# Performance work log

Hardware: AMD Instinct MI355X
Metric: run time of the kernel (lower is better)

Reference implementation:

```python
import jax, jax.numpy as jnp
import numpy as np

B, N, C = 32, 577, 768
H = 12
DH = C // H  # 64
SCALE = DH ** -0.5


def setup_inputs() -> dict:
    key = jax.random.key(0)
    ks = jax.random.split(key, 5)
    x = jax.random.normal(ks[0], (B, N, C), dtype=jnp.float32)
    # Linear params (torch convention: y = x @ W.T + b)
    qkv_w = jax.random.normal(ks[1], (3 * C, C), dtype=jnp.float32) * (C ** -0.5)
    qkv_b = jnp.zeros((3 * C,), dtype=jnp.float32)
    proj_w = jax.random.normal(ks[2], (C, C), dtype=jnp.float32) * (C ** -0.5)
    proj_b = jnp.zeros((C,), dtype=jnp.float32)
    return {"x": x, "qkv_w": qkv_w, "qkv_b": qkv_b, "proj_w": proj_w, "proj_b": proj_b}


def reference(x, qkv_w, qkv_b, proj_w, proj_b):
    b, n, c = x.shape
    qkv = x @ qkv_w.T + qkv_b                       # [B, N, 3C]
    qkv = qkv.reshape(b, n, 3, H, DH).transpose(2, 0, 3, 1, 4)  # [3, B, H, N, DH]
    q, k, v = qkv[0], qkv[1], qkv[2]
    q = q * SCALE
    attn = jnp.einsum('bhnd,bhmd->bhnm', q, k)      # [B, H, N, N]
    # sigmoid -> inverse-sigmoid straight-through rewrite (forward equals logit(sigmoid(attn)))
    sig = jax.nn.sigmoid(attn)
    inv_sig = jnp.log(sig / (1.0 - sig))
    attn_st = attn + jax.lax.stop_gradient(inv_sig - attn)
    p = jax.nn.softmax(attn_st, axis=-1)
    out = jnp.einsum('bhnm,bhmd->bhnd', p, v)       # [B, H, N, DH]
    out = out.transpose(0, 2, 1, 3).reshape(b, n, c)
    return out @ proj_w.T + proj_b
```

## Files before the change

kernel.cpp:

```cpp
#include <hip/hip_runtime.h>

typedef __bf16 bf16;
typedef __attribute__((ext_vector_type(4))) __bf16 bf16x4;
typedef __attribute__((ext_vector_type(8))) __bf16 bf16x8;
typedef __attribute__((ext_vector_type(4))) float f32x4;

#define MFMA_BF16(A_, B_, C_) __builtin_amdgcn_mfma_f32_16x16x32_bf16(A_, B_, C_, 0, 0, 0)

#define BB    32
#define SEQ   577
#define CH    768
#define NH    12
#define DHD   64
#define MROWS (BB * SEQ)
#define NQKV  2304
#define SEQP  584
#define QSCALE 0.1803368801111204f

#define NSTEP 24

__device__ __forceinline__ int xcd_chunk(int bid, int nwg) {
  int q8 = nwg >> 3, r8 = nwg & 7;
  int xcd = bid & 7, sub = bid >> 3;
  return (xcd < r8 ? xcd * (q8 + 1) : r8 * (q8 + 1) + (xcd - r8) * q8) + sub;
}

__device__ __forceinline__ void async_ld16(const bf16* g, bf16* l) {
  __builtin_amdgcn_global_load_lds(
      (const __attribute__((address_space(1))) void*)g,
      (__attribute__((address_space(3))) void*)l, 16, 0, 0);
}

__global__ __launch_bounds__(256) void cvt_bf16(const float* __restrict__ src,
                                                bf16* __restrict__ dst, int n) {
  int idx = (blockIdx.x * 256 + threadIdx.x) * 4;
  if (idx >= n) return;
  float4 v = *(const float4*)(src + idx);
  bf16x4 o = {(bf16)v.x, (bf16)v.y, (bf16)v.z, (bf16)v.w};
  *(bf16x4*)(dst + idx) = o;
}

__global__ __launch_bounds__(256) void pad_v(bf16* __restrict__ vt) {
  int r = blockIdx.x * 256 + threadIdx.x;
  if (r < BB * NH * DHD) {
    bf16* p = vt + (size_t)r * SEQP + SEQ;
#pragma unroll
    for (int i = 0; i < 7; ++i) p[i] = (bf16)0.f;
  }
}

__global__ __launch_bounds__(256, 2)
void gemm_qkv(const bf16* __restrict__ A, const bf16* __restrict__ W,
              const float* __restrict__ bias,
              bf16* __restrict__ qrm, bf16* __restrict__ krm, bf16* __restrict__ vt) {
  __shared__ bf16 As[2][128 * 32];
  __shared__ bf16 Bs[2][128 * 32];
  const int tid = threadIdx.x, lane = tid & 63, wid = tid >> 6;
  const int quad = lane >> 4, r15 = lane & 15;
  const int m0 = blockIdx.y * 128, n0 = blockIdx.x * 128;
  const int waveM = wid & 1, waveN = wid >> 1;

  const bf16* aSrc[2];
  const bf16* bSrc[2];
  for (int c = 0; c < 2; ++c) {
    int q = wid * 128 + c * 64 + lane;
    int row = q >> 2;
    int sw = (row ^ (row >> 2)) & 3;
    int kc = (q & 3) ^ sw;
    aSrc[c] = A + (size_t)(m0 + row) * CH + kc * 8;
    bSrc[c] = W + (size_t)(n0 + row) * CH + kc * 8;
  }

  f32x4 acc[4][4];
#pragma unroll
  for (int i = 0; i < 4; ++i)
#pragma unroll
    for (int j = 0; j < 4; ++j) acc[i][j] = (f32x4){0.f, 0.f, 0.f, 0.f};

#define GSTAGE(K0, BUF)                                                   \
  {                                                                       \
    _Pragma("unroll") for (int c = 0; c < 2; ++c) {                       \
      async_ld16(aSrc[c] + (K0), &As[BUF][(wid * 128 + c * 64) * 8]);     \
      async_ld16(bSrc[c] + (K0), &Bs[BUF][(wid * 128 + c * 64) * 8]);     \
    }                                                                     \
  }

#define GCOMPUTE(BUF)                                                     \
  {                                                                       \
    bf16x8 af[4], bfr[4];                                                 \
    _Pragma("unroll") for (int s = 0; s < 4; ++s) {                       \
      int rowA = waveM * 64 + s * 16 + r15;                               \
      int ca = quad ^ ((rowA ^ (rowA >> 2)) & 3);                         \
      af[s] = *(const bf16x8*)(&As[BUF][rowA * 32 + ca * 8]);             \
      int rowB = waveN * 64 + s * 16 + r15;                               \
      int cb = quad ^ ((rowB ^ (rowB >> 2)) & 3);                         \
      bfr[s] = *(const bf16x8*)(&Bs[BUF][rowB * 32 + cb * 8]);            \
    }                                                                     \
    _Pragma("unroll") for (int sm = 0; sm < 4; ++sm)                      \
      _Pragma("unroll") for (int sn = 0; sn < 4; ++sn)                    \
        acc[sm][sn] = MFMA_BF16(af[sm], bfr[sn], acc[sm][sn]);            \
  }

  GSTAGE(0, 0);
  for (int k0 = 0; k0 < CH; k0 += 64) {
    __syncthreads();
    GSTAGE(k0 + 32, 1);
    GCOMPUTE(0);
    __syncthreads();
    if (k0 + 64 < CH) GSTAGE(k0 + 64, 0);
    GCOMPUTE(1);
  }

  int t = (n0 >= 1536) ? 2 : (n0 >= 768 ? 1 : 0);
#pragma unroll
  for (int sn = 0; sn < 4; ++sn) {
    int gn = n0 + waveN * 64 + sn * 16 + r15;
    float bv = bias[gn];
    int col = gn - t * CH;
    int h = col >> 6, d = col & 63;
#pragma unroll
    for (int sm = 0; sm < 4; ++sm) {
      int gmBase = m0 + waveM * 64 + sm * 16 + quad * 4;
#pragma unroll
      for (int r = 0; r < 4; ++r) {
        int gm = gmBase + r;
        if (gm < MROWS) {
          float v = acc[sm][sn][r] + bv;
          if (t == 0) {
            qrm[(size_t)gm * CH + col] = (bf16)(v * QSCALE);
          } else if (t == 1) {
            krm[(size_t)gm * CH + col] = (bf16)v;
          } else {
            int b_ = gm / SEQ;
            int n_ = gm - b_ * SEQ;
            vt[((size_t)(b_ * NH + h) * DHD + d) * SEQP + n_] = (bf16)v;
          }
        }
      }
    }
  }
}
#undef GSTAGE
#undef GCOMPUTE

__global__ __launch_bounds__(512, 2)
void gemm_proj(const bf16* __restrict__ A, const bf16* __restrict__ W,
               const float* __restrict__ bias, float* __restrict__ out) {
  __shared__ bf16 As[4][256 * 32];
  __shared__ bf16 Bs[4][256 * 32];
  const int tid = threadIdx.x, lane = tid & 63, wid = tid >> 6;
  const int quad = lane >> 4, r15 = lane & 15;

  const int nbx = (int)gridDim.x;
  const int wg = xcd_chunk((int)blockIdx.y * nbx + (int)blockIdx.x,
                           nbx * (int)gridDim.y);
  const int m0 = (wg / nbx) * 256, n0 = (wg % nbx) * 256;

  const int rm = (wid >> 2) * 128;
  const int rn = (wid & 3) * 64;

  int aOff[2], bOff[2];
#pragma unroll
  for (int i = 0; i < 2; ++i) {
    int slot = i * 512 + tid;
    int row = slot >> 2, pc2 = slot & 3;
    int gc2 = pc2 ^ ((row ^ (row >> 2)) & 3);
    aOff[i] = (m0 + row) * CH + gc2 * 8;
    bOff[i] = (n0 + row) * CH + gc2 * 8;
  }

  f32x4 acc[8][4];
#pragma unroll
  for (int i = 0; i < 8; ++i)
#pragma unroll
    for (int j = 0; j < 4; ++j) acc[i][j] = (f32x4){0.f, 0.f, 0.f, 0.f};

#define ISSUE2(S)                                                              \
  {                                                                            \
    const int kb_ = (S) * 32;                                                  \
    const int bf_ = (S) & 3;                                                   \
    _Pragma("unroll") for (int i = 0; i < 2; ++i) {                            \
      async_ld16(A + aOff[i] + kb_, &As[bf_][(i * 512 + tid) * 8]);            \
      async_ld16(W + bOff[i] + kb_, &Bs[bf_][(i * 512 + tid) * 8]);            \
    }                                                                          \
  }

#define COMPUTE2(BF)                                                           \
  {                                                                            \
    bf16x8 bfr[4], afr[8];                                                     \
    _Pragma("unroll") for (int sn = 0; sn < 4; ++sn) {                         \
      int fr = rn + sn * 16 + r15;                                             \
      int pc2 = quad ^ ((fr ^ (fr >> 2)) & 3);                                 \
      bfr[sn] = *(const bf16x8*)(&Bs[BF][fr * 32 + pc2 * 8]);                  \
    }                                                                          \
    _Pragma("unroll") for (int sm = 0; sm < 8; ++sm) {                         \
      int fr = rm + sm * 16 + r15;                                             \
      int pc2 = quad ^ ((fr ^ (fr >> 2)) & 3);                                 \
      afr[sm] = *(const bf16x8*)(&As[BF][fr * 32 + pc2 * 8]);                  \
    }                                                                          \
    _Pragma("unroll") for (int sm = 0; sm < 8; ++sm)                           \
      _Pragma("unroll") for (int sn = 0; sn < 4; ++sn)                         \
        acc[sm][sn] = MFMA_BF16(afr[sm], bfr[sn], acc[sm][sn]);                \
  }

  ISSUE2(0);
  ISSUE2(1);
  for (int s = 0; s < NSTEP; ++s) {
    if (s < NSTEP - 2) {
      ISSUE2(s + 2);
      asm volatile("s_waitcnt vmcnt(8)" ::: "memory");
    } else if (s == NSTEP - 2) {
      asm volatile("s_waitcnt vmcnt(4)" ::: "memory");
    } else {
      asm volatile("s_waitcnt vmcnt(0)" ::: "memory");
    }
    __builtin_amdgcn_s_barrier();
    asm volatile("" ::: "memory");
    COMPUTE2(s & 3);
  }

#pragma unroll
  for (int sn = 0; sn < 4; ++sn) {
    int gn = n0 + rn + sn * 16 + r15;
    float bv = bias[gn];
#pragma unroll
    for (int sm = 0; sm < 8; ++sm) {
      int gmBase = m0 + rm + sm * 16 + quad * 4;
#pragma unroll
      for (int r = 0; r < 4; ++r) {
        int gm = gmBase + r;
        if (gm < MROWS) out[(size_t)gm * CH + gn] = acc[sm][sn][r] + bv;
      }
    }
  }
}
#undef ISSUE2
#undef COMPUTE2

__global__ __launch_bounds__(256, 3)
void attn_kernel(const bf16* __restrict__ qrm, const bf16* __restrict__ krm,
                 const bf16* __restrict__ vt, bf16* __restrict__ ob) {
  __shared__ bf16 Ks[2][128 * 32];
  __shared__ bf16 Vt[2][128 * 32];
  __shared__ bf16 Ps[4][2][16 * 72];
  const int tid = threadIdx.x, lane = tid & 63, wid = tid >> 6;
  const int quad = lane >> 4, r15 = lane & 15;
  const int nbx = (int)gridDim.x;
  const int wg = xcd_chunk((int)blockIdx.y * nbx + (int)blockIdx.x,
                           nbx * (int)gridDim.y);
  const int qt = wg % nbx, bh = wg / nbx;
  const int b_ = bh / NH, h = bh - b_ * NH;
  const bf16* vtb = vt + (size_t)bh * DHD * SEQP;
  const bf16* krmb = krm + (size_t)b_ * SEQ * CH + h * DHD;

  int jloc_[2], off_[2];
  const bf16* kp_[2];
  const bf16* vp_[2];
#pragma unroll
  for (int c = 0; c < 2; ++c) {
    int q = wid * 128 + c * 64 + lane;
    int hr = q >> 2;
    int kc = (q & 3) ^ ((hr ^ (hr >> 2)) & 3);
    jloc_[c] = hr >> 1;
    off_[c] = (hr & 1) * 32 + kc * 8;
    kp_[c] = krmb + (size_t)jloc_[c] * CH + off_[c];
    vp_[c] = vtb + (size_t)jloc_[c] * SEQP + off_[c];
  }

#define ASTAGE_CLEAN(BUF)                                                      \
  {                                                                            \
    _Pragma("unroll") for (int c = 0; c < 2; ++c) {                            \
      async_ld16(kp_[c], &Ks[BUF][(wid * 128 + c * 64) * 8]);                  \
      async_ld16(vp_[c], &Vt[BUF][(wid * 128 + c * 64) * 8]);                  \
      kp_[c] += 64 * CH;                                                       \
      vp_[c] += 64;                                                            \
    }                                                                          \
  }

#define ASTAGE_TAIL(BUF)                                                       \
  {                                                                            \
    _Pragma("unroll") for (int c = 0; c < 2; ++c) {                            \
      async_ld16(krmb + (size_t)(SEQ - 1) * CH + off_[c],                      \
                 &Ks[BUF][(wid * 128 + c * 64) * 8]);                          \
      async_ld16(vtb + (size_t)jloc_[c] * SEQP + (SEQ - 1),                    \
                 &Vt[BUF][(wid * 128 + c * 64) * 8]);                          \
    }                                                                          \
  }

  bf16x8 qf[2][2];
#pragma unroll
  for (int g = 0; g < 2; ++g) {
    int qrow = qt * 128 + wid * 32 + g * 16 + r15;
    if (qrow > SEQ - 1) qrow = SEQ - 1;
    const bf16* qp = qrm + (size_t)(b_ * SEQ + qrow) * CH + h * DHD + quad * 8;
    qf[g][0] = *(const bf16x8*)qp;
    qf[g][1] = *(const bf16x8*)(qp + 32);
  }

  f32x4 oacc[2][4];
#pragma unroll
  for (int g = 0; g < 2; ++g)
#pragma unroll
    for (int i = 0; i < 4; ++i) oacc[g][i] = (f32x4){0.f, 0.f, 0.f, 0.f};
  float lrow0 = 0.f, lrow1 = 0.f;

  bf16* P0 = &Ps[wid][0][0];
  bf16* P1 = &Ps[wid][1][0];

#define QKT_PV(BUF, MASKED)                                                    \
  {                                                                            \
    f32x4 s0[4], s1[4];                                                        \
    _Pragma("unroll") for (int sj = 0; sj < 4; ++sj) {                         \
      int hr0 = (sj * 16 + r15) * 2, hr1 = hr0 + 1;                            \
      int p0c = quad ^ ((hr0 ^ (hr0 >> 2)) & 3);                               \
      int p1c = quad ^ ((hr1 ^ (hr1 >> 2)) & 3);                               \
      bf16x8 kf0 = *(const bf16x8*)(&Ks[BUF][hr0 * 32 + p0c * 8]);             \
      bf16x8 kf1 = *(const bf16x8*)(&Ks[BUF][hr1 * 32 + p1c * 8]);             \
      f32x4 z = (f32x4){0.f, 0.f, 0.f, 0.f};                                   \
      s0[sj] = MFMA_BF16(kf0, qf[0][0], z);                                    \
      s0[sj] = MFMA_BF16(kf1, qf[0][1], s0[sj]);                               \
      s1[sj] = MFMA_BF16(kf0, qf[1][0], z);                                    \
      s1[sj] = MFMA_BF16(kf1, qf[1][1], s1[sj]);                               \
    }                                                                          \
    _Pragma("unroll") for (int sj = 0; sj < 4; ++sj)                           \
      _Pragma("unroll") for (int r = 0; r < 4; ++r) {                          \
        float e0, e1;                                                          \
        if (MASKED) {                                                          \
          bool ok = (sj == 0) && (quad == 0) && (r == 0);     \
          e0 = ok ? __builtin_amdgcn_exp2f(s0[sj][r]) : 0.f;                   \
          e1 = ok ? __builtin_amdgcn_exp2f(s1[sj][r]) : 0.f;                   \
        } else {                                                               \
          e0 = __builtin_amdgcn_exp2f(s0[sj][r]);                              \
          e1 = __builtin_amdgcn_exp2f(s1[sj][r]);                              \
        }                                                                      \
        s0[sj][r] = e0; lrow0 += e0;                                           \
        s1[sj][r] = e1; lrow1 += e1;                                           \
      }                                                                        \
    _Pragma("unroll") for (int sj = 0; sj < 4; ++sj) {                         \
      bf16x4 p0 = {(bf16)s0[sj][0], (bf16)s0[sj][1],                           \
                   (bf16)s0[sj][2], (bf16)s0[sj][3]};                          \
      bf16x4 p1 = {(bf16)s1[sj][0], (bf16)s1[sj][1],                           \
                   (bf16)s1[sj][2], (bf16)s1[sj][3]};                          \
      *(bf16x4*)(P0 + r15 * 72 + sj * 16 + quad * 4) = p0;                     \
      *(bf16x4*)(P1 + r15 * 72 + sj * 16 + quad * 4) = p1;                     \
    }                                                                          \
    asm volatile("s_waitcnt lgkmcnt(0)" ::: "memory");   \
    _Pragma("unroll") for (int kc = 0; kc < 2; ++kc) {                         \
      bf16x8 pf0 = *(const bf16x8*)(P0 + r15 * 72 + kc * 32 + quad * 8);       \
      bf16x8 pf1 = *(const bf16x8*)(P1 + r15 * 72 + kc * 32 + quad * 8);       \
      _Pragma("unroll") for (int sd = 0; sd < 4; ++sd) {                       \
        int hrv = (sd * 16 + r15) * 2 + kc;                                    \
        int pv = quad ^ ((hrv ^ (hrv >> 2)) & 3);                              \
        bf16x8 vf = *(const bf16x8*)(&Vt[BUF][hrv * 32 + pv * 8]);             \
        oacc[0][sd] = MFMA_BF16(pf0, vf, oacc[0][sd]);                         \
        oacc[1][sd] = MFMA_BF16(pf1, vf, oacc[1][sd]);                         \
      }                                                                        \
    }                                                                          \
  }

  ASTAGE_CLEAN(0);
  int buf = 0;
  for (int t = 0; t < 9; ++t) {
    __syncthreads();
    if (t < 8) { ASTAGE_CLEAN(buf ^ 1); } else { ASTAGE_TAIL(buf ^ 1); }
    QKT_PV(buf, 0);
    buf ^= 1;
  }
  __syncthreads();
  QKT_PV(buf, 1);
#undef ASTAGE_CLEAN
#undef ASTAGE_TAIL
#undef QKT_PV

  lrow0 += __shfl_xor(lrow0, 16);
  lrow0 += __shfl_xor(lrow0, 32);
  lrow1 += __shfl_xor(lrow1, 16);
  lrow1 += __shfl_xor(lrow1, 32);

#pragma unroll
  for (int g = 0; g < 2; ++g) {
    float lr = (g == 0) ? lrow0 : lrow1;
#pragma unroll
    for (int r = 0; r < 4; ++r) {
      int m = quad * 4 + r;
      float rs = __shfl(lr, m);
      int orow = qt * 128 + wid * 32 + g * 16 + m;
      if (orow < SEQ) {
        float inv = 1.0f / rs;
        size_t rowoff = ((size_t)(b_ * SEQ + orow)) * CH + h * DHD;
#pragma unroll
        for (int sd = 0; sd < 4; ++sd)
          ob[rowoff + sd * 16 + r15] = (bf16)(oacc[g][sd][r] * inv);
      }
    }
  }
}

extern "C" void kernel_launch(void* const* d_in, const int* in_sizes, int n_in,
                              void* d_out, int out_size, void* d_ws, size_t ws_size,
                              hipStream_t stream) {
  const float* x      = (const float*)d_in[0];
  const float* qkv_w  = (const float*)d_in[1];
  const float* qkv_b  = (const float*)d_in[2];
  const float* proj_w = (const float*)d_in[3];
  const float* proj_b = (const float*)d_in[4];
  float* out = (float*)d_out;

  char* w = (char*)d_ws;
  bf16* xb  = (bf16*)(w);
  bf16* wqp = (bf16*)(w + 28360704);
  bf16* qrm = (bf16*)(w + 31899648);
  bf16* krm = (bf16*)(w + 60260352);
  bf16* vtb = (bf16*)(w + 88621056);

  cvt_bf16<<<(MROWS * CH / 4 + 255) / 256, 256, 0, stream>>>(x, xb, MROWS * CH);
  cvt_bf16<<<(NQKV * CH / 4 + 255) / 256, 256, 0, stream>>>(qkv_w, wqp, NQKV * CH);
  pad_v<<<(BB * NH * DHD + 255) / 256, 256, 0, stream>>>(vtb);

  gemm_qkv<<<dim3(NQKV / 128, 145), 256, 0, stream>>>(
      xb, wqp, qkv_b, qrm, krm, vtb);

  attn_kernel<<<dim3(5, BB * NH), 256, 0, stream>>>(qrm, krm, vtb, xb);

  cvt_bf16<<<(CH * CH / 4 + 255) / 256, 256, 0, stream>>>(proj_w, wqp, CH * CH);

  gemm_proj<<<dim3(CH / 256, 73), 512, 0, stream>>>(xb, wqp, proj_b, out);
}
```

Baseline: 344.3 us.

## Triple-buffer QKV GEMM with vmcnt-based prefetch and XCD-aware tile mapping

Replaces the double-buffered K loop in the QKV projection GEMM with a three-stage ring. Loads are issued two steps ahead and each step waits with an explicit s_waitcnt vmcnt plus one barrier, instead of two full __syncthreads per pair of steps. Workgroup IDs are also remapped through xcd_chunk so neighbouring tiles land on the same XCD for L2 reuse. The launch bound is raised to 3 blocks per CU. The extra LDS buffer and the tighter register budget could limit occupancy or cause spills. The hand-written vmcnt counts also depend on the compiler issuing exactly four async loads per stage.

Result: no change. 348.3 us (+1.2%).

```diff
diff --git a/kernel.cpp b/kernel.cpp
--- a/kernel.cpp
+++ b/kernel.cpp
@@ -49,15 +49,18 @@
   }
 }
 
-__global__ __launch_bounds__(256, 2)
+__global__ __launch_bounds__(256, 3)
 void gemm_qkv(const bf16* __restrict__ A, const bf16* __restrict__ W,
               const float* __restrict__ bias,
               bf16* __restrict__ qrm, bf16* __restrict__ krm, bf16* __restrict__ vt) {
-  __shared__ bf16 As[2][128 * 32];
-  __shared__ bf16 Bs[2][128 * 32];
+  __shared__ bf16 As[3][128 * 32];
+  __shared__ bf16 Bs[3][128 * 32];
   const int tid = threadIdx.x, lane = tid & 63, wid = tid >> 6;
   const int quad = lane >> 4, r15 = lane & 15;
-  const int m0 = blockIdx.y * 128, n0 = blockIdx.x * 128;
+  const int nbx = (int)gridDim.x;
+  const int wg = xcd_chunk((int)blockIdx.y * nbx + (int)blockIdx.x,
+                           nbx * (int)gridDim.y);
+  const int m0 = (wg / nbx) * 128, n0 = (wg % nbx) * 128;
   const int waveM = wid & 1, waveN = wid >> 1;
 
   const bf16* aSrc[2];
@@ -77,38 +80,44 @@
 #pragma unroll
     for (int j = 0; j < 4; ++j) acc[i][j] = (f32x4){0.f, 0.f, 0.f, 0.f};
 
-#define GSTAGE(K0, BUF)                                                   \
+#define QISSUE(S)                                                         \
   {                                                                       \
+    const int kb_ = (S) * 32;                                             \
+    const int bf_ = (S) % 3;                                              \
     _Pragma("unroll") for (int c = 0; c < 2; ++c) {                       \
-      async_ld16(aSrc[c] + (K0), &As[BUF][(wid * 128 + c * 64) * 8]);     \
-      async_ld16(bSrc[c] + (K0), &Bs[BUF][(wid * 128 + c * 64) * 8]);     \
+      async_ld16(aSrc[c] + kb_, &As[bf_][(wid * 128 + c * 64) * 8]);      \
+      async_ld16(bSrc[c] + kb_, &Bs[bf_][(wid * 128 + c * 64) * 8]);      \
     }                                                                     \
   }
 
-#define GCOMPUTE(BUF)                                                     \
+#define QCOMPUTE(BF)                                                      \
   {                                                                       \
     bf16x8 af[4], bfr[4];                                                 \
-    _Pragma("unroll") for (int s = 0; s < 4; ++s) {                       \
-      int rowA = waveM * 64 + s * 16 + r15;                               \
+    _Pragma("unroll") for (int s_ = 0; s_ < 4; ++s_) {                    \
+      int rowA = waveM * 64 + s_ * 16 + r15;                              \
       int ca = quad ^ ((rowA ^ (rowA >> 2)) & 3);                         \
-      af[s] = *(const bf16x8*)(&As[BUF][rowA * 32 + ca * 8]);             \
-      int rowB = waveN * 64 + s * 16 + r15;                               \
+      af[s_] = *(const bf16x8*)(&As[BF][rowA * 32 + ca * 8]);             \
+      int rowB = waveN * 64 + s_ * 16 + r15;                              \
       int cb = quad ^ ((rowB ^ (rowB >> 2)) & 3);                         \
-      bfr[s] = *(const bf16x8*)(&Bs[BUF][rowB * 32 + cb * 8]);            \
+      bfr[s_] = *(const bf16x8*)(&Bs[BF][rowB * 32 + cb * 8]);            \
     }                                                                     \
     _Pragma("unroll") for (int sm = 0; sm < 4; ++sm)                      \
       _Pragma("unroll") for (int sn = 0; sn < 4; ++sn)                    \
         acc[sm][sn] = MFMA_BF16(af[sm], bfr[sn], acc[sm][sn]);            \
   }
 
-  GSTAGE(0, 0);
-  for (int k0 = 0; k0 < CH; k0 += 64) {
-    __syncthreads();
-    GSTAGE(k0 + 32, 1);
-    GCOMPUTE(0);
-    __syncthreads();
-    if (k0 + 64 < CH) GSTAGE(k0 + 64, 0);
-    GCOMPUTE(1);
+  QISSUE(0);
+  QISSUE(1);
+  for (int s = 0; s < NSTEP; ++s) {
+    if (s < NSTEP - 1) {
+      asm volatile("s_waitcnt vmcnt(4)" ::: "memory");
+    } else {
+      asm volatile("s_waitcnt vmcnt(0)" ::: "memory");
+    }
+    __builtin_amdgcn_s_barrier();
+    asm volatile("" ::: "memory");
+    if (s < NSTEP - 2) QISSUE(s + 2);
+    QCOMPUTE(s % 3);
   }
 
   int t = (n0 >= 1536) ? 2 : (n0 >= 768 ? 1 : 0);
@@ -140,8 +149,8 @@
     }
   }
 }
-#undef GSTAGE
-#undef GCOMPUTE
+#undef QISSUE
+#undef QCOMPUTE
 
 __global__ __launch_bounds__(512, 2)
 void gemm_proj(const bf16* __restrict__ A, const bf16* __restrict__ W,
```
